# Optimization experiments

Measured on AMD Instinct MI355X. Metric: run time of the kernel, lower is better.

Reference implementation:

```python
import jax, jax.numpy as jnp
import numpy as np

# ---- config (YOLOv4-style, TRAIN_SIZE=608, P2..P5) ----
STRIDES = (4.0, 8.0, 16.0, 32.0)
ANCHORS = np.array([
    [[12, 16], [19, 36], [40, 28], [36, 75]],
    [[36, 75], [76, 55], [72, 146], [142, 110]],
    [[72, 146], [142, 110], [192, 243], [459, 401]],
    [[142, 110], [192, 243], [300, 300], [459, 401]],
], dtype=np.float32)  # [LEVELS, NUM_ANCHORS, 2]
MAX_PROP = 100
SCORE_THRESH = 0.25
IOU_THRESH = 0.5


def decode_prediction(p, anchors, stride):
    # p: [b, A, h, w, 6] -> [b, A*h*w, 5] with xyxy + score
    b, A, h, w, _ = p.shape
    txy, twh, conf, cls = p[..., :2], p[..., 2:4], p[..., 4:5], p[..., 5:6]
    gx, gy = jnp.meshgrid(jnp.arange(w, dtype=p.dtype), jnp.arange(h, dtype=p.dtype))
    grid = jnp.stack([gx, gy], axis=-1)[None, None]  # [1,1,h,w,2]
    xy = (jax.nn.sigmoid(txy) + grid) * stride
    wh = jnp.exp(twh) * anchors[None, :, None, None, :]
    score = jax.nn.sigmoid(conf) * jax.nn.sigmoid(cls)
    x1y1 = xy - 0.5 * wh
    x2y2 = xy + 0.5 * wh
    out = jnp.concatenate([x1y1, x2y2, score], axis=-1)  # [b,A,h,w,5]
    return out.reshape(b, A * h * w, 5)


def _iou_one_vs_all(box, boxes):
    # box: [4], boxes: [N,4] (xyxy)
    lt = jnp.maximum(box[:2], boxes[:, :2])
    rb = jnp.minimum(box[2:], boxes[:, 2:])
    wh = jnp.maximum(rb - lt, 0.0)
    inter = wh[:, 0] * wh[:, 1]
    a1 = jnp.maximum(box[2] - box[0], 0.0) * jnp.maximum(box[3] - box[1], 0.0)
    a2 = jnp.maximum(boxes[:, 2] - boxes[:, 0], 0.0) * jnp.maximum(boxes[:, 3] - boxes[:, 1], 0.0)
    return inter / (a1 + a2 - inter + 1e-9)


def _nms_single(boxes, scores):
    # greedy NMS, padded to MAX_PROP with zero rows
    s0 = jnp.where(scores >= SCORE_THRESH, scores, 0.0)

    def step(s, _):
        i = jnp.argmax(s)
        sc = s[i]
        box = boxes[i]
        keep = sc > 0.0
        row = jnp.where(keep, jnp.concatenate([box, sc[None]]), jnp.zeros(5, boxes.dtype))
        iou = _iou_one_vs_all(box, boxes)
        s = jnp.where((iou > IOU_THRESH) & keep, 0.0, s)
        s = s.at[i].set(0.0)
        return s, row

    _, props = jax.lax.scan(step, s0, None, length=MAX_PROP)
    return props  # [MAX_PROP, 5]


def entry_stop_gradients(t, mask):
    # gradient flows only through entries where mask==1
    return jax.lax.stop_gradient(t) * (1.0 - mask) + t * mask


def _forward(p2, p3, p4, p5):
    anchors = jnp.asarray(ANCHORS)
    d2 = decode_prediction(p2, anchors[0], STRIDES[0])
    d3 = decode_prediction(p3, anchors[1], STRIDES[1])
    d4 = decode_prediction(p4, anchors[2], STRIDES[2])
    d5 = decode_prediction(p5, anchors[3], STRIDES[3])
    proposals = jnp.concatenate([d2, d3, d4, d5], axis=1)  # [b, N, 5]
    proposals = jax.vmap(lambda pr: _nms_single(pr[:, :4], pr[:, 4]))(proposals)  # [b, MAX_PROP, 5]
    mask = (jnp.sum(proposals[..., :4], axis=-1) != 0.0).astype(proposals.dtype)[..., None]
    return entry_stop_gradients(proposals, mask)


def setup_inputs() -> dict:
    key = jax.random.key(0)
    k2, k3, k4, k5 = jax.random.split(key, 4)
    b, A, ch = 32, 4, 6
    return {
        "p2": jax.random.normal(k2, (b, A, 152, 152, ch), dtype=jnp.float32),
        "p3": jax.random.normal(k3, (b, A, 76, 76, ch), dtype=jnp.float32),
        "p4": jax.random.normal(k4, (b, A, 38, 38, ch), dtype=jnp.float32),
        "p5": jax.random.normal(k5, (b, A, 19, 19, ch), dtype=jnp.float32),
    }


def reference(p2, p3, p4, p5):
    return _forward(p2, p3, p4, p5)
```

## Files before the change

### kernel.cpp

```cpp
#include <hip/hip_runtime.h>
#include <cstdint>
#include <cstddef>

typedef unsigned int u32;
typedef unsigned long long u64;

#define NTOT 122740
#define NQ   30685
#define NPAIR 61370
#define KTOP 1024
#define WIN  256
#define NBIN 4096
#define SCORE_T 0.25f
#define TBITS 0x3E800000u
#define CSTRIDE 64


#define WS_COUNTERS 524288
#define WS_COMPACT  532480
#define WS_SCORES   794624

__device__ __forceinline__ float sigm(float x) { return 1.0f / (1.0f + expf(-x)); }

__device__ __forceinline__ int score_bin(u32 bits) {
  return min(4095, 1 + (int)((bits - TBITS) >> 12));
}

__device__ __forceinline__ u64 shfl_xor_u64(u64 x, int m) {
  int lo = __shfl_xor((int)(u32)x, m, 64);
  int hi = __shfl_xor((int)(u32)(x >> 32), m, 64);
  return ((u64)(u32)hi << 32) | (u32)lo;
}

__device__ float4 decode_box_from_gidx(u32 gidx, int b,
    const float* __restrict__ p2, const float* __restrict__ p3,
    const float* __restrict__ p4, const float* __restrict__ p5)
{
  const float* p; int t, H, W; float stride;
  float aw0, ah0, aw1, ah1, aw2, ah2, aw3, ah3;
  if (gidx < 92416u) {
    p = p2 + (size_t)b * 92416 * 6; t = (int)gidx; H = 152; W = 152; stride = 4.0f;
    aw0=12.f; ah0=16.f; aw1=19.f; ah1=36.f; aw2=40.f; ah2=28.f; aw3=36.f; ah3=75.f;
  } else if (gidx < 115520u) {
    p = p3 + (size_t)b * 23104 * 6; t = (int)(gidx - 92416u); H = 76; W = 76; stride = 8.0f;
    aw0=36.f; ah0=75.f; aw1=76.f; ah1=55.f; aw2=72.f; ah2=146.f; aw3=142.f; ah3=110.f;
  } else if (gidx < 121296u) {
    p = p4 + (size_t)b * 5776 * 6; t = (int)(gidx - 115520u); H = 38; W = 38; stride = 16.0f;
    aw0=72.f; ah0=146.f; aw1=142.f; ah1=110.f; aw2=192.f; ah2=243.f; aw3=459.f; ah3=401.f;
  } else {
    p = p5 + (size_t)b * 1444 * 6; t = (int)(gidx - 121296u); H = 19; W = 19; stride = 32.0f;
    aw0=142.f; ah0=110.f; aw1=192.f; ah1=243.f; aw2=300.f; ah2=300.f; aw3=459.f; ah3=401.f;
  }
  int HW = H * W;
  int a = t / HW;
  int r = t - a * HW;
  int y = r / W;
  int x = r - y * W;
  const float* q = p + (size_t)t * 6;
  float2 t01 = *(const float2*)(q + 0);
  float2 t23 = *(const float2*)(q + 2);
  float cx = (sigm(t01.x) + (float)x) * stride;
  float cy = (sigm(t01.y) + (float)y) * stride;
  float aw = (a == 0) ? aw0 : (a == 1) ? aw1 : (a == 2) ? aw2 : aw3;
  float ah = (a == 0) ? ah0 : (a == 1) ? ah1 : (a == 2) ? ah2 : ah3;
  float bw = expf(t23.x) * aw;
  float bh = expf(t23.y) * ah;
  return make_float4(cx - 0.5f * bw, cy - 0.5f * bh, cx + 0.5f * bw, cy + 0.5f * bh);
}

__device__ __forceinline__ bool iou_gt(float4 A, float4 B) {
  float ltx = fmaxf(A.x, B.x), lty = fmaxf(A.y, B.y);
  float rbx = fminf(A.z, B.z), rby = fminf(A.w, B.w);
  float w = fmaxf(rbx - ltx, 0.0f), h = fmaxf(rby - lty, 0.0f);
  float inter = w * h;
  float a1 = fmaxf(A.z - A.x, 0.0f) * fmaxf(A.w - A.y, 0.0f);
  float a2 = fmaxf(B.z - B.x, 0.0f) * fmaxf(B.w - B.y, 0.0f);
  float iou = inter / (a1 + a2 - inter + 1e-9f);
  return iou > 0.5f;
}

__global__ __launch_bounds__(1024)
void zero_kernel(u32* w) {
  int t = blockIdx.x * 1024 + threadIdx.x;
  if (t < 133120) w[t] = 0u;
}

__global__ __launch_bounds__(256)
void decode_score_hist(const float* __restrict__ p2, const float* __restrict__ p3,
                       const float* __restrict__ p4, const float* __restrict__ p5,
                       u32* __restrict__ scores, u32* __restrict__ hist)
{
  __shared__ u32 lhist[NBIN];
  const int tid = threadIdx.x;
  const int b = blockIdx.y;
  for (int i = tid; i < NBIN; i += 256) lhist[i] = 0u;
  __syncthreads();

  uint2* srow = (uint2*)(scores + (size_t)b * NTOT);
  const int pbase = blockIdx.x * 2048;
  #pragma unroll 2
  for (int k = 0; k < 8; ++k) {
    int P = pbase + k * 256 + tid;
    if (P < NPAIR) {
      int t0 = 2 * P;
      const float* p; int l0, LN;
      if (t0 < 92416)       { p = p2; l0 = t0;          LN = 92416; }
      else if (t0 < 115520) { p = p3; l0 = t0 - 92416;  LN = 23104; }
      else if (t0 < 121296) { p = p4; l0 = t0 - 115520; LN = 5776;  }
      else                  { p = p5; l0 = t0 - 121296; LN = 1444;  }
      const float* q = p + ((size_t)b * LN + (size_t)l0) * 6 + 4;
      float4 v1 = *(const float4*)(q);
      float4 v2 = *(const float4*)(q + 4);
      float s0 = sigm(v1.x) * sigm(v1.y);
      float s1 = sigm(v2.z) * sigm(v2.w);
      u32 b0 = (s0 >= SCORE_T) ? __float_as_uint(s0) : 0u;
      u32 b1 = (s1 >= SCORE_T) ? __float_as_uint(s1) : 0u;
      srow[P] = make_uint2(b0, b1);
      if (b0) atomicAdd(&lhist[score_bin(b0)], 1u);
      if (b1) atomicAdd(&lhist[score_bin(b1)], 1u);
    }
  }
  __syncthreads();
  u32* gh = hist + (size_t)b * NBIN;
  for (int i = tid; i < NBIN; i += 256) {
    u32 v = lhist[i];
    if (v) atomicAdd(&gh[i], v);
  }
}

__global__ __launch_bounds__(256)
void filter_kernel(const u32* __restrict__ scores, const u32* __restrict__ hist,
                   u32* __restrict__ counters, uint2* __restrict__ compact)
{
  __shared__ u32 shist[NBIN];
  __shared__ u32 scan[256];
  __shared__ uint2 cand[KTOP];
  __shared__ u32 s_cnt, s_base;
  __shared__ int s_B;
  const int tid = threadIdx.x;
  const int b = blockIdx.y;

  const u32* gh = hist + (size_t)b * NBIN;
  for (int i = tid; i < NBIN; i += 256) shist[i] = gh[i];
  if (tid == 0) s_cnt = 0u;
  __syncthreads();

  u32 g = 0;
  const int base = tid * 16;
  #pragma unroll
  for (int k = 0; k < 16; ++k) g += shist[base + k];
  scan[tid] = g;
  __syncthreads();
  for (int off = 1; off < 256; off <<= 1) {
    u32 v = (tid + off < 256) ? scan[tid + off] : 0u;
    __syncthreads();
    scan[tid] += v;
    __syncthreads();
  }
  if (tid == 0 && scan[0] <= (u32)KTOP) s_B = 1;
  {
    u32 nxt = (tid < 255) ? scan[tid + 1] : 0u;
    if (scan[tid] > (u32)KTOP && nxt <= (u32)KTOP) {
      u32 c = nxt;
      int Bv = base + 16;
      for (int bin = base + 15; bin >= base; --bin) {
        c += shist[bin];
        if (c <= (u32)KTOP) Bv = bin; else break;
      }
      s_B = Bv;
    }
  }
  __syncthreads();
  const int B = max(s_B, 1);

  const uint4* sp = (const uint4*)(scores + (size_t)b * NTOT);
  const int i0 = blockIdx.x * 2048;
  const int i1 = min(i0 + 2048, NQ);
  for (int i = i0 + tid; i < i1; i += 256) {
    uint4 v = sp[i];
    u32 c4[4] = { v.x, v.y, v.z, v.w };
    #pragma unroll
    for (int c = 0; c < 4; ++c) {
      u32 bits = c4[c];
      if (bits && score_bin(bits) >= B) {
        u32 pos = atomicAdd(&s_cnt, 1u);
        if (pos < (u32)KTOP) cand[pos] = make_uint2(bits, (u32)(4 * i + c));
      }
    }
  }
  __syncthreads();
  const u32 m = min(s_cnt, (u32)KTOP);
  if (tid == 0) s_base = m ? atomicAdd(&counters[(size_t)b * CSTRIDE], m) : 0u;
  __syncthreads();
  const u32 gbase = s_base;
  uint2* crow = compact + (size_t)b * KTOP;
  for (u32 i = tid; i < m; i += 256) {
    u32 dst = gbase + i;
    if (dst < (u32)KTOP) crow[dst] = cand[i];
  }
}

__global__ __launch_bounds__(1024, 1)
void sort_nms_kernel(const uint2* __restrict__ compact, const u32* __restrict__ counters,
                     const float* __restrict__ p2, const float* __restrict__ p3,
                     const float* __restrict__ p4, const float* __restrict__ p5,
                     float* __restrict__ out)
{
  const int b = blockIdx.x;
  const int tid = threadIdx.x;

  __shared__ u64 skey[KTOP];
  __shared__ float4 sbox[WIN];
  __shared__ u64 smat[WIN * 4];
  __shared__ float4 selbox[100];
  __shared__ int s_misc[4];

  const int n = min((int)counters[(size_t)b * CSTRIDE], KTOP);
  const uint2* crow = compact + (size_t)b * KTOP;

  u64 v;
  if (tid < n) {
    uint2 pr = crow[tid];
    v = ~(((u64)pr.x << 32) | (u32)(~pr.y));
  } else {
    v = ~0ull;
  }

  for (int kk = 2; kk <= KTOP; kk <<= 1) {
    for (int jj = kk >> 1; jj > 0; jj >>= 1) {
      u64 w;
      if (jj >= 64) {
        skey[tid] = v;
        __syncthreads();
        w = skey[tid ^ jj];
        __syncthreads();
      } else {
        w = shfl_xor_u64(v, jj);
      }
      bool keep_min = (((tid & kk) == 0) == ((tid & jj) == 0));
      u64 mn = (v < w) ? v : w;
      u64 mx = (v < w) ? w : v;
      v = keep_min ? mn : mx;
    }
  }
  skey[tid] = v;
  __syncthreads();

  const int Wn = min(n, WIN);

  if (tid < WIN) {
    sbox[tid] = (tid < Wn) ? decode_box_from_gidx(~(u32)(~skey[tid]), b, p2, p3, p4, p5)
                           : make_float4(0.f, 0.f, 0.f, 0.f);
  }
  __syncthreads();

  {
    int row = tid >> 2, word = tid & 3;
    u64 bits = 0;
    if (row < Wn) {
      float4 A = sbox[row];
      int j0 = word * 64;
      int je = min(64, Wn - j0);
      for (int j = 0; j < je; ++j)
        if (iou_gt(A, sbox[j0 + j])) bits |= (1ull << j);
    }
    smat[tid] = bits;
  }
  __syncthreads();

  if (tid == 0) {
    u64 live[4];
    #pragma unroll
    for (int w2 = 0; w2 < 4; ++w2) {
      int lo = w2 * 64;
      live[w2] = (Wn >= lo + 64) ? ~0ull : (Wn > lo ? ((1ull << (Wn - lo)) - 1ull) : 0ull);
    }
    int sel = 0;
    #pragma unroll 1
    for (int w2 = 0; w2 < 4; ++w2) {
      while (live[w2] && sel < 100) {
        int j = (int)__ffsll((unsigned long long)live[w2]) - 1;
        int p = (w2 << 6) + j;
        u64 r0 = smat[p * 4 + 0];
        u64 r1 = smat[p * 4 + 1];
        u64 r2 = smat[p * 4 + 2];
        u64 r3 = smat[p * 4 + 3];
        float4 box = sbox[p];
        u64 kcomp = ~skey[p];
        float sc = __uint_as_float((u32)(kcomp >> 32));
        selbox[sel] = box;
        float* orow = out + (size_t)b * 500 + (size_t)sel * 5;
        orow[0] = box.x; orow[1] = box.y; orow[2] = box.z; orow[3] = box.w; orow[4] = sc;
        sel++;
        live[0] &= ~r0; live[1] &= ~r1; live[2] &= ~r2; live[3] &= ~r3;
        live[w2] &= ~(1ull << j);
      }
    }
    s_misc[2] = sel;
    s_misc[3] = (sel < 100 && n > WIN) ? 1 : 0;
  }
  __syncthreads();

  if (s_misc[3]) {
    if (tid < 64) {
      const int lane = tid;
      int sel = s_misc[2];
      for (int p = WIN; p < n && sel < 100; ++p) {
        u64 kcomp = ~skey[p];
        float4 box = decode_box_from_gidx(~(u32)kcomp, b, p2, p3, p4, p5);
        bool hit = false;
        if (lane < sel) hit = iou_gt(selbox[lane], box);
        if (lane + 64 < sel) hit = hit || iou_gt(selbox[lane + 64], box);
        u64 anyhit = __ballot(hit);
        if (anyhit == 0ull) {
          if (lane == 0) {
            selbox[sel] = box;
            float sc = __uint_as_float((u32)(kcomp >> 32));
            float* orow = out + (size_t)b * 500 + (size_t)sel * 5;
            orow[0] = box.x; orow[1] = box.y; orow[2] = box.z; orow[3] = box.w; orow[4] = sc;
          }
          sel++;
        }
      }
      if (lane == 0) s_misc[2] = sel;
    }
  }
  __syncthreads();

  const int nsel = s_misc[2];
  for (int i = tid; i < (100 - nsel) * 5; i += 1024)
    out[(size_t)b * 500 + (size_t)nsel * 5 + i] = 0.0f;
}

extern "C" void kernel_launch(void* const* d_in, const int* in_sizes, int n_in,
                              void* d_out, int out_size, void* d_ws, size_t ws_size,
                              hipStream_t stream) {
  const float* p2 = (const float*)d_in[0];
  const float* p3 = (const float*)d_in[1];
  const float* p4 = (const float*)d_in[2];
  const float* p5 = (const float*)d_in[3];
  float* out = (float*)d_out;

  unsigned char* w = (unsigned char*)d_ws;
  u32*   hist     = (u32*)w;
  u32*   counters = (u32*)(w + WS_COUNTERS);
  uint2* compact  = (uint2*)(w + WS_COMPACT);
  u32*   scores   = (u32*)(w + WS_SCORES);

  zero_kernel<<<130, 1024, 0, stream>>>(hist);
  decode_score_hist<<<dim3(30, 32), 256, 0, stream>>>(p2, p3, p4, p5, scores, hist);
  filter_kernel<<<dim3(15, 32), 256, 0, stream>>>(scores, hist, counters, compact);
  sort_nms_kernel<<<32, 1024, 0, stream>>>(compact, counters, p2, p3, p4, p5, out);
}
```

Measured before the change: 181.7 us.

## Bucket candidates by histogram bin offsets and replace bitonic sort with odd-even pass

Adds a separate scan kernel that turns each batch's score histogram into per-bin exclusive offsets and stores the count and threshold bin. The filter kernel then scatters candidates straight into bin-ordered slots with per-bin global atomics, so the compacted list is already roughly sorted and the shared-memory staging and per-block base atomic go away. The sort kernel swaps the full bitonic network for an odd-even transposition sort with early exit, which only pays off when the input is nearly sorted, though it can take up to 600 barrier-heavy rounds. NMS selection now runs on a full wavefront with suppression rows kept in registers and fetched by shuffles, instead of a single thread reading shared memory.

```diff
diff --git a/kernel.cpp b/kernel.cpp
--- a/kernel.cpp
+++ b/kernel.cpp
@@ -26,9 +26,9 @@
   return min(4095, 1 + (int)((bits - TBITS) >> 12));
 }
 
-__device__ __forceinline__ u64 shfl_xor_u64(u64 x, int m) {
-  int lo = __shfl_xor((int)(u32)x, m, 64);
-  int hi = __shfl_xor((int)(u32)(x >> 32), m, 64);
+__device__ __forceinline__ u64 shfl_u64(u64 x, int src) {
+  int lo = __shfl((int)(u32)x, src, 64);
+  int hi = __shfl((int)(u32)(x >> 32), src, 64);
   return ((u64)(u32)hi << 32) | (u32)lo;
 }
 
@@ -129,26 +129,22 @@
 }
 
 __global__ __launch_bounds__(256)
-void filter_kernel(const u32* __restrict__ scores, const u32* __restrict__ hist,
-                   u32* __restrict__ counters, uint2* __restrict__ compact)
+void scan_kernel(u32* __restrict__ hist, u32* __restrict__ counters)
 {
   __shared__ u32 shist[NBIN];
   __shared__ u32 scan[256];
-  __shared__ uint2 cand[KTOP];
-  __shared__ u32 s_cnt, s_base;
-  __shared__ int s_B;
+  __shared__ int s_B, s_n;
   const int tid = threadIdx.x;
-  const int b = blockIdx.y;
-
-  const u32* gh = hist + (size_t)b * NBIN;
+  const int b = blockIdx.x;
+  u32* gh = hist + (size_t)b * NBIN;
   for (int i = tid; i < NBIN; i += 256) shist[i] = gh[i];
-  if (tid == 0) s_cnt = 0u;
-  __syncthreads();
-
+  __syncthreads();
+
+  u32 loc[16];
   u32 g = 0;
   const int base = tid * 16;
   #pragma unroll
-  for (int k = 0; k < 16; ++k) g += shist[base + k];
+  for (int k = 0; k < 16; ++k) { loc[k] = shist[base + k]; g += loc[k]; }
   scan[tid] = g;
   __syncthreads();
   for (int off = 1; off < 256; off <<= 1) {
@@ -157,22 +153,38 @@
     scan[tid] += v;
     __syncthreads();
   }
-  if (tid == 0 && scan[0] <= (u32)KTOP) s_B = 1;
+  if (tid == 0 && scan[0] <= (u32)KTOP) { s_B = 1; s_n = (int)scan[0]; }
   {
     u32 nxt = (tid < 255) ? scan[tid + 1] : 0u;
     if (scan[tid] > (u32)KTOP && nxt <= (u32)KTOP) {
-      u32 c = nxt;
-      int Bv = base + 16;
-      for (int bin = base + 15; bin >= base; --bin) {
-        c += shist[bin];
-        if (c <= (u32)KTOP) Bv = bin; else break;
+      u32 c = nxt; int Bv = base + 16; u32 nv = nxt;
+      for (int k = 15; k >= 0; --k) {
+        c += loc[k];
+        if (c <= (u32)KTOP) { Bv = base + k; nv = c; } else break;
       }
-      s_B = Bv;
-    }
-  }
-  __syncthreads();
-  const int B = max(s_B, 1);
-
+      s_B = Bv; s_n = (int)nv;
+    }
+  }
+  {
+    u32 s = (tid < 255) ? scan[tid + 1] : 0u;
+    for (int k = 15; k >= 0; --k) { gh[base + k] = s; s += loc[k]; }
+  }
+  __syncthreads();
+  if (tid == 0) {
+    counters[(size_t)b * CSTRIDE]     = (u32)s_n;
+    counters[(size_t)b * CSTRIDE + 1] = (u32)max(s_B, 1);
+  }
+}
+
+__global__ __launch_bounds__(256)
+void filter_kernel(const u32* __restrict__ scores, u32* __restrict__ binpos,
+                   const u32* __restrict__ counters, uint2* __restrict__ compact)
+{
+  const int tid = threadIdx.x;
+  const int b = blockIdx.y;
+  const int B = (int)counters[(size_t)b * CSTRIDE + 1];
+  u32* bp = binpos + (size_t)b * NBIN;
+  uint2* crow = compact + (size_t)b * KTOP;
   const uint4* sp = (const uint4*)(scores + (size_t)b * NTOT);
   const int i0 = blockIdx.x * 2048;
   const int i1 = min(i0 + 2048, NQ);
@@ -182,21 +194,15 @@
     #pragma unroll
     for (int c = 0; c < 4; ++c) {
       u32 bits = c4[c];
-      if (bits && score_bin(bits) >= B) {
-        u32 pos = atomicAdd(&s_cnt, 1u);
-        if (pos < (u32)KTOP) cand[pos] = make_uint2(bits, (u32)(4 * i + c));
+      if (bits) {
+        int bin = score_bin(bits);
+        if (bin >= B) {
+          u32 slot = atomicAdd(&bp[bin], 1u);
+          if (slot < (u32)KTOP)
+            crow[slot] = make_uint2(bits, (u32)(4 * i + c));
+        }
       }
     }
-  }
-  __syncthreads();
-  const u32 m = min(s_cnt, (u32)KTOP);
-  if (tid == 0) s_base = m ? atomicAdd(&counters[(size_t)b * CSTRIDE], m) : 0u;
-  __syncthreads();
-  const u32 gbase = s_base;
-  uint2* crow = compact + (size_t)b * KTOP;
-  for (u32 i = tid; i < m; i += 256) {
-    u32 dst = gbase + i;
-    if (dst < (u32)KTOP) crow[dst] = cand[i];
   }
 }
 
@@ -214,48 +220,49 @@
   __shared__ u64 smat[WIN * 4];
   __shared__ float4 selbox[100];
   __shared__ int s_misc[4];
+  __shared__ int s_flag;
 
   const int n = min((int)counters[(size_t)b * CSTRIDE], KTOP);
   const uint2* crow = compact + (size_t)b * KTOP;
 
-  u64 v;
   if (tid < n) {
     uint2 pr = crow[tid];
-    v = ~(((u64)pr.x << 32) | (u32)(~pr.y));
+    skey[tid] = ((u64)pr.x << 32) | (u32)(~pr.y);
   } else {
-    v = ~0ull;
-  }
-
-  for (int kk = 2; kk <= KTOP; kk <<= 1) {
-    for (int jj = kk >> 1; jj > 0; jj >>= 1) {
-      u64 w;
-      if (jj >= 64) {
-        skey[tid] = v;
-        __syncthreads();
-        w = skey[tid ^ jj];
-        __syncthreads();
-      } else {
-        w = shfl_xor_u64(v, jj);
-      }
-      bool keep_min = (((tid & kk) == 0) == ((tid & jj) == 0));
-      u64 mn = (v < w) ? v : w;
-      u64 mx = (v < w) ? w : v;
-      v = keep_min ? mn : mx;
-    }
-  }
-  skey[tid] = v;
-  __syncthreads();
+    skey[tid] = 0ull;
+  }
+  __syncthreads();
+
+  for (int round = 0; round < 600; ++round) {
+    if (tid == 0) s_flag = 0;
+    __syncthreads();
+    if (tid < 512) {
+      int p = 2 * tid;
+      u64 a = skey[p], c = skey[p + 1];
+      if (a < c) { skey[p] = c; skey[p + 1] = a; s_flag = 1; }
+    }
+    __syncthreads();
+    if (tid < 511) {
+      int p = 2 * tid + 1;
+      u64 a = skey[p], c = skey[p + 1];
+      if (a < c) { skey[p] = c; skey[p + 1] = a; s_flag = 1; }
+    }
+    __syncthreads();
+    int f = s_flag;
+    __syncthreads();
+    if (!f) break;
+  }
 
   const int Wn = min(n, WIN);
 
   if (tid < WIN) {
-    sbox[tid] = (tid < Wn) ? decode_box_from_gidx(~(u32)(~skey[tid]), b, p2, p3, p4, p5)
+    sbox[tid] = (tid < Wn) ? decode_box_from_gidx(~(u32)skey[tid], b, p2, p3, p4, p5)
                            : make_float4(0.f, 0.f, 0.f, 0.f);
   }
   __syncthreads();
 
   {
-    int row = tid >> 2, word = tid & 3;
+    int row = tid & 255, word = tid >> 8;
     u64 bits = 0;
     if (row < Wn) {
       float4 A = sbox[row];
@@ -264,40 +271,54 @@
       for (int j = 0; j < je; ++j)
         if (iou_gt(A, sbox[j0 + j])) bits |= (1ull << j);
     }
-    smat[tid] = bits;
-  }
-  __syncthreads();
-
-  if (tid == 0) {
+    smat[word * 256 + row] = bits;
+  }
+  __syncthreads();
+
+  if (tid < 64) {
+    const int lane = tid;
+    u64 m0[4], m1[4], m2[4], m3[4];
+    #pragma unroll
+    for (int w = 0; w < 4; ++w) {
+      m0[w] = smat[w * 256 +   0 + lane];
+      m1[w] = smat[w * 256 +  64 + lane];
+      m2[w] = smat[w * 256 + 128 + lane];
+      m3[w] = smat[w * 256 + 192 + lane];
+    }
     u64 live[4];
     #pragma unroll
-    for (int w2 = 0; w2 < 4; ++w2) {
-      int lo = w2 * 64;
-      live[w2] = (Wn >= lo + 64) ? ~0ull : (Wn > lo ? ((1ull << (Wn - lo)) - 1ull) : 0ull);
+    for (int g2 = 0; g2 < 4; ++g2) {
+      int lo = g2 * 64;
+      live[g2] = (Wn >= lo + 64) ? ~0ull : (Wn > lo ? ((1ull << (Wn - lo)) - 1ull) : 0ull);
     }
     int sel = 0;
     #pragma unroll 1
     for (int w2 = 0; w2 < 4; ++w2) {
       while (live[w2] && sel < 100) {
-        int j = (int)__ffsll((unsigned long long)live[w2]) - 1;
+        int j = (int)__ffsll(live[w2]) - 1;
         int p = (w2 << 6) + j;
-        u64 r0 = smat[p * 4 + 0];
-        u64 r1 = smat[p * 4 + 1];
-        u64 r2 = smat[p * 4 + 2];
-        u64 r3 = smat[p * 4 + 3];
-        float4 box = sbox[p];
-        u64 kcomp = ~skey[p];
-        float sc = __uint_as_float((u32)(kcomp >> 32));
-        selbox[sel] = box;
-        float* orow = out + (size_t)b * 500 + (size_t)sel * 5;
-        orow[0] = box.x; orow[1] = box.y; orow[2] = box.z; orow[3] = box.w; orow[4] = sc;
-        sel++;
+        u64 r0, r1, r2, r3;
+        if (w2 == 0)      { r0 = shfl_u64(m0[0], j); r1 = shfl_u64(m0[1], j); r2 = shfl_u64(m0[2], j); r3 = shfl_u64(m0[3], j); }
+        else if (w2 == 1) { r0 = shfl_u64(m1[0], j); r1 = shfl_u64(m1[1], j); r2 = shfl_u64(m1[2], j); r3 = shfl_u64(m1[3], j); }
+        else if (w2 == 2) { r0 = shfl_u64(m2[0], j); r1 = shfl_u64(m2[1], j); r2 = shfl_u64(m2[2], j); r3 = shfl_u64(m2[3], j); }
+        else              { r0 = shfl_u64(m3[0], j); r1 = shfl_u64(m3[1], j); r2 = shfl_u64(m3[2], j); r3 = shfl_u64(m3[3], j); }
         live[0] &= ~r0; live[1] &= ~r1; live[2] &= ~r2; live[3] &= ~r3;
         live[w2] &= ~(1ull << j);
+        if (lane == 0) {
+          float4 box = sbox[p];
+          u64 k = skey[p];
+          float sc = __uint_as_float((u32)(k >> 32));
+          selbox[sel] = box;
+          float* orow = out + (size_t)b * 500 + (size_t)sel * 5;
+          orow[0] = box.x; orow[1] = box.y; orow[2] = box.z; orow[3] = box.w; orow[4] = sc;
+        }
+        sel++;
       }
     }
-    s_misc[2] = sel;
-    s_misc[3] = (sel < 100 && n > WIN) ? 1 : 0;
+    if (lane == 0) {
+      s_misc[2] = sel;
+      s_misc[3] = (sel < 100 && n > WIN) ? 1 : 0;
+    }
   }
   __syncthreads();
 
@@ -306,8 +327,8 @@
       const int lane = tid;
       int sel = s_misc[2];
       for (int p = WIN; p < n && sel < 100; ++p) {
-        u64 kcomp = ~skey[p];
-        float4 box = decode_box_from_gidx(~(u32)kcomp, b, p2, p3, p4, p5);
+        u64 k = skey[p];
+        float4 box = decode_box_from_gidx(~(u32)k, b, p2, p3, p4, p5);
         bool hit = false;
         if (lane < sel) hit = iou_gt(selbox[lane], box);
         if (lane + 64 < sel) hit = hit || iou_gt(selbox[lane + 64], box);
@@ -315,7 +336,7 @@
         if (anyhit == 0ull) {
           if (lane == 0) {
             selbox[sel] = box;
-            float sc = __uint_as_float((u32)(kcomp >> 32));
+            float sc = __uint_as_float((u32)(k >> 32));
             float* orow = out + (size_t)b * 500 + (size_t)sel * 5;
             orow[0] = box.x; orow[1] = box.y; orow[2] = box.z; orow[3] = box.w; orow[4] = sc;
           }
@@ -349,6 +370,7 @@
 
   zero_kernel<<<130, 1024, 0, stream>>>(hist);
   decode_score_hist<<<dim3(30, 32), 256, 0, stream>>>(p2, p3, p4, p5, scores, hist);
+  scan_kernel<<<32, 256, 0, stream>>>(hist, counters);
   filter_kernel<<<dim3(15, 32), 256, 0, stream>>>(scores, hist, counters, compact);
   sort_nms_kernel<<<32, 1024, 0, stream>>>(compact, counters, p2, p3, p4, p5, out);
 }
```

Measured after the change: 189.7 us. 1.04x slower.
